# Performance work log

Measured on AMD Instinct MI355X. Metric: run time of the kernel, lower is better.

## Reference

```python
import jax, jax.numpy as jnp
from jax import lax
import numpy as np

EPS = 1e-5


def ref_points(Hk, Wk):
    # torch linspace(0.5, Hk-0.5, Hk)/Hk * 2 - 1, stacked (y, x)
    ys = (jnp.linspace(0.5, Hk - 0.5, Hk) / Hk) * 2.0 - 1.0
    xs = (jnp.linspace(0.5, Wk - 0.5, Wk) / Wk) * 2.0 - 1.0
    yy, xx = jnp.meshgrid(ys, xs, indexing='ij')
    return jnp.stack([yy, xx], axis=-1)  # (Hk, Wk, 2) in (y, x) order


def grid_sample(img, grid):
    # Bilinear, align_corners=True, zeros padding (torch F.grid_sample defaults).
    # img: (N, C, Hi, Wi); grid: (N, Hg, Wg, 2) with (x, y) in [-1, 1].
    N, C, Hi, Wi = img.shape
    Hg, Wg = grid.shape[1], grid.shape[2]
    gx = (grid[..., 0] + 1.0) * 0.5 * (Wi - 1)
    gy = (grid[..., 1] + 1.0) * 0.5 * (Hi - 1)
    x0 = jnp.floor(gx)
    y0 = jnp.floor(gy)
    wx1 = gx - x0
    wy1 = gy - y0
    imgf = img.reshape(N, C, Hi * Wi)

    def corner(ix, iy, w):
        valid = (ix >= 0) & (ix < Wi) & (iy >= 0) & (iy < Hi)
        idx = (jnp.clip(iy, 0, Hi - 1).astype(jnp.int32) * Wi
               + jnp.clip(ix, 0, Wi - 1).astype(jnp.int32)).reshape(N, -1)
        vals = jax.vmap(lambda im, f: im[:, f])(imgf, idx)  # (N, C, Hg*Wg)
        return vals * (w * valid).reshape(N, 1, -1)

    out = (corner(x0, y0, (1 - wx1) * (1 - wy1))
           + corner(x0 + 1, y0, wx1 * (1 - wy1))
           + corner(x0, y0 + 1, (1 - wx1) * wy1)
           + corner(x0 + 1, y0 + 1, wx1 * wy1))
    return out.reshape(N, C, Hg, Wg)


def setup_inputs() -> dict:
    key = jax.random.key(0)
    ks = jax.random.split(key, 8)
    B, C, H, W = 8, 128, 64, 64
    gc, nH = 64, 4
    return {
        'x': jax.random.normal(ks[0], (B, C, H, W), jnp.float32),
        'w_dw': jax.random.normal(ks[1], (gc, 1, 5, 5), jnp.float32) * 0.1,
        'ln_w': jnp.ones((gc,), jnp.float32),
        'w_off': jax.random.normal(ks[2], (3, gc), jnp.float32) * 0.1,
        'wq': jax.random.normal(ks[3], (C, C), jnp.float32) * 0.05,
        'wk': jax.random.normal(ks[4], (C, C), jnp.float32) * 0.05,
        'wv': jax.random.normal(ks[5], (C, C), jnp.float32) * 0.05,
        'wo': jax.random.normal(ks[6], (C, C), jnp.float32) * 0.05,
        'rpe': jax.random.normal(ks[7], (nH, 2 * H - 1, 2 * W - 1), jnp.float32) * 0.01,
    }


def reference(x, w_dw, ln_w, w_off, wq, wk, wv, wo, rpe):
    B, C, H, W = x.shape
    G, nH = 2, 4
    gc = C // G           # group channels
    dh = C // nH          # head channels
    gh = nH // G          # heads per group
    scale = dh ** -0.5
    orf = 1.0             # offset_range_factor

    conv1x1 = lambda t, w: jnp.einsum('oi,bihw->bohw', w, t)

    q = conv1x1(x, wq)                                    # (B, C, H, W)
    q_off = q.reshape(B * G, gc, H, W)

    # conv_offset: depthwise 5x5 stride 4 pad 2 -> BiasFree LN (over C) -> GELU -> 1x1 to 3
    off = lax.conv_general_dilated(q_off, w_dw, (4, 4), ((2, 2), (2, 2)),
                                   dimension_numbers=('NCHW', 'OIHW', 'NCHW'),
                                   feature_group_count=gc)  # (B*G, gc, Hk, Wk)
    var = jnp.var(off, axis=1, keepdims=True)
    off = off / jnp.sqrt(var + EPS) * ln_w.reshape(1, -1, 1, 1)
    off = jax.nn.gelu(off, approximate=False)
    off = jnp.einsum('oi,bihw->bohw', w_off, off)          # (B*G, 3, Hk, Wk)

    Hk, Wk = off.shape[2], off.shape[3]
    n = Hk * Wk

    # channel 0 = y offset, channel 1 = x offset, channel 2 = modulation
    offset = jnp.stack([jnp.tanh(off[:, 0]) * (orf / Hk),
                        jnp.tanh(off[:, 1]) * (orf / Wk)], axis=-1)  # (B*G, Hk, Wk, 2) (y,x)
    dm = jax.nn.sigmoid(off[:, 2])[:, None]                # (B*G, 1, Hk, Wk)

    pos = offset + ref_points(Hk, Wk)[None]                # (B*G, Hk, Wk, 2) (y,x)

    xs = grid_sample(x.reshape(B * G, gc, H, W), pos[..., ::-1])  # grid in (x,y)
    xs = (xs * dm).reshape(B, C, 1, n)

    k = conv1x1(xs, wk).reshape(B * nH, dh, n)
    v = conv1x1(xs, wv).reshape(B * nH, dh, n)
    qf = q.reshape(B * nH, dh, H * W)

    attn = jnp.einsum('bcm,bcn->bmn', qf, k) * scale       # (B*nH, H*W, n)

    # relative-position bias sampled at continuous displacements
    rpe_b = jnp.broadcast_to(rpe[None], (B, nH, 2 * H - 1, 2 * W - 1)
                             ).reshape(B * G, gh, 2 * H - 1, 2 * W - 1)
    qg = ref_points(H, W).reshape(H * W, 2)                # (H*W, 2)
    disp = (qg[None, :, None, :] - pos.reshape(B * G, 1, n, 2)) * 0.5  # (B*G, H*W, n, 2)
    bias = grid_sample(rpe_b, disp[..., ::-1]).reshape(B * nH, H * W, n)

    attn = jax.nn.softmax(attn + bias, axis=2)
    out = jnp.einsum('bmn,bcn->bcm', attn, v).reshape(B, C, H, W)
    return conv1x1(out, wo)
```

## Files before the change

kernel.cpp:

```cpp
#include <hip/hip_runtime.h>
#include <hip/hip_bf16.h>
#include <math.h>

#define HW 4096
#define NCH 128

typedef __attribute__((ext_vector_type(8))) short short8;
typedef __attribute__((ext_vector_type(4))) float f32x4;
typedef __attribute__((ext_vector_type(4))) unsigned u32x4;

__device__ __forceinline__ short f2bf(float f) {
  union { __hip_bfloat16 h; short s; } u;
  u.h = __float2bfloat16(f);
  return u.s;
}
__device__ __forceinline__ float bf2f(short s) {
  union { unsigned u; float f; } u;
  u.u = ((unsigned)(unsigned short)s) << 16;
  return u.f;
}

__global__ __launch_bounds__(256) void xq_kernel(
    const float* __restrict__ x, const float* __restrict__ wq,
    short* __restrict__ xT, float* __restrict__ qT) {
  __shared__ float s[128][65];
  int tid = threadIdx.x;
  int b = blockIdx.y;
  int m0 = blockIdx.x * 64;
  {
    int ml = tid & 63, ch = tid >> 6;
#pragma unroll
    for (int i = 0; i < 32; ++i) {
      int c = i * 4 + ch;
      s[c][ml] = x[((size_t)(b * NCH + c)) * HW + m0 + ml];
    }
  }
  __syncthreads();
  {
    int c = tid & 127, mh = tid >> 7;
#pragma unroll
    for (int i = 0; i < 32; ++i) {
      int m = i * 2 + mh;
      xT[((size_t)(b * HW + m0 + m)) * NCH + c] = f2bf(s[c][m]);
    }
  }
  int w = tid >> 6, lane = tid & 63, l15 = lane & 15, qd = lane >> 4;
  int mrow = w * 16 + l15;
  f32x4 acc[8];
#pragma unroll
  for (int ot = 0; ot < 8; ++ot) acc[ot] = (f32x4){0.f, 0.f, 0.f, 0.f};
#pragma unroll
  for (int kc = 0; kc < 4; ++kc) {
    short8 ah, al;
#pragma unroll
    for (int j = 0; j < 8; ++j) {
      float v = s[kc * 32 + qd * 8 + j][mrow];
      short hi = f2bf(v);
      ah[j] = hi;
      al[j] = f2bf(v - bf2f(hi));
    }
#pragma unroll
    for (int ot = 0; ot < 8; ++ot) {
      const float* wr = wq + (size_t)(ot * 16 + l15) * NCH + kc * 32 + qd * 8;
      f32x4 w0 = *(const f32x4*)wr;
      f32x4 w1 = *(const f32x4*)(wr + 4);
      short8 bh, bl;
#pragma unroll
      for (int j = 0; j < 4; ++j) {
        short h0 = f2bf(w0[j]);
        bh[j] = h0;
        bl[j] = f2bf(w0[j] - bf2f(h0));
        short h1 = f2bf(w1[j]);
        bh[4 + j] = h1;
        bl[4 + j] = f2bf(w1[j] - bf2f(h1));
      }
      acc[ot] = __builtin_amdgcn_mfma_f32_16x16x32_bf16(ah, bh, acc[ot], 0, 0, 0);
      acc[ot] = __builtin_amdgcn_mfma_f32_16x16x32_bf16(al, bh, acc[ot], 0, 0, 0);
      acc[ot] = __builtin_amdgcn_mfma_f32_16x16x32_bf16(ah, bl, acc[ot], 0, 0, 0);
    }
  }
#pragma unroll
  for (int ot = 0; ot < 8; ++ot)
#pragma unroll
    for (int r = 0; r < 4; ++r)
      qT[((size_t)(b * HW + m0 + w * 16 + qd * 4 + r)) * NCH + ot * 16 + l15] =
          acc[ot][r];
}

__device__ __forceinline__ float wsum64(float v) {
#pragma unroll
  for (int o = 32; o > 0; o >>= 1) v += __shfl_xor(v, o);
  return v;
}

__global__ __launch_bounds__(256) void conv_offset_kernel(
    const float* __restrict__ qT, const float* __restrict__ w_dw,
    const float* __restrict__ ln_w, const float* __restrict__ w_off,
    const float* __restrict__ wk, const float* __restrict__ wv,
    const float* __restrict__ wo, const float* __restrict__ rpe,
    float* __restrict__ pos, float* __restrict__ dm,
    short* __restrict__ wk_bf, short* __restrict__ wv_bf,
    short* __restrict__ wo_bf, unsigned* __restrict__ tab) {
  int tid = threadIdx.x;
  if (blockIdx.x >= 64) {
    int id = (blockIdx.x - 64) * 16 + blockIdx.y;
    if (id < 64) {
      int i = id * 256 + tid;
      wk_bf[i] = f2bf(wk[i]);
      wv_bf[i] = f2bf(wv[i]);
      wo_bf[i] = f2bf(wo[i]);
    } else {
      int i = (id - 64) * 256 + tid;
      int h = i >> 14, r = i & 16383;
      int row = r >> 7, col = r & 127;
      float lo = 0.f, hi = 0.f;
      if (col < 127) {
        if (row >= 1) lo = rpe[h * 16129 + (row - 1) * 127 + col];
        if (row < 127) hi = rpe[h * 16129 + row * 127 + col];
      }
      union { unsigned u; _Float16 h2[2]; } pk;
      pk.h2[0] = (_Float16)(lo * 1.4426950408889634f);
      pk.h2[1] = (_Float16)(hi * 1.4426950408889634f);
      tab[i] = pk.u;
    }
    return;
  }
  int c = tid & 63;
  int p = blockIdx.x * 4 + (tid >> 6);
  int bg = blockIdx.y;
  int py = p >> 4, px = p & 15;
  const float* qp = qT + (size_t)(bg >> 1) * HW * NCH + (bg & 1) * 64 + c;
  const float* wd = w_dw + c * 25;
  float acc = 0.f;
#pragma unroll
  for (int ky = 0; ky < 5; ++ky) {
    int iy = 4 * py + ky - 2;
    if (iy < 0 || iy >= 64) continue;
#pragma unroll
    for (int kx = 0; kx < 5; ++kx) {
      int ix = 4 * px + kx - 2;
      if (ix < 0 || ix >= 64) continue;
      acc += wd[ky * 5 + kx] * qp[(size_t)(iy * 64 + ix) * NCH];
    }
  }
  float mean = wsum64(acc) * (1.f / 64.f);
  float msq = wsum64(acc * acc) * (1.f / 64.f);
  float var = msq - mean * mean;
  float g = acc * rsqrtf(var + 1e-5f) * ln_w[c];
  g = 0.5f * g * (1.f + erff(g * 0.70710678118654752f));
  float o0 = wsum64(w_off[c] * g);
  float o1 = wsum64(w_off[64 + c] * g);
  float o2 = wsum64(w_off[128 + c] * g);
  if (c == 0) {
    int idx = bg * 256 + p;
    pos[idx * 2] = tanhf(o0) * (1.f / 16.f) + ((py + 0.5f) * (1.f / 8.f) - 1.f);
    pos[idx * 2 + 1] = tanhf(o1) * (1.f / 16.f) + ((px + 0.5f) * (1.f / 8.f) - 1.f);
    dm[idx] = 1.f / (1.f + expf(-o2));
  }
}

__global__ __launch_bounds__(256) void sample_xs_kernel(
    const short* __restrict__ xT, const float* __restrict__ pos,
    const float* __restrict__ dm, short* __restrict__ xsT) {
  int tid = threadIdx.x;
  int c = tid & 63;
  int p = blockIdx.y * 4 + (tid >> 6);
  int bg = blockIdx.x;
  int b = bg >> 1, ch0 = (bg & 1) * 64;
  int idx = bg * 256 + p;
  float posy = pos[idx * 2], posx = pos[idx * 2 + 1];
  float dmv = dm[idx];
  float gx = (posx + 1.f) * 31.5f;
  float gy = (posy + 1.f) * 31.5f;
  float x0f = floorf(gx), y0f = floorf(gy);
  int ix = (int)x0f, iy = (int)y0f;
  float fx = gx - x0f, fy = gy - y0f;
  float w00 = (1.f - fx) * (1.f - fy), w10 = fx * (1.f - fy);
  float w01 = (1.f - fx) * fy, w11 = fx * fy;
  bool vx0 = (ix >= 0 && ix < 64), vx1 = (ix + 1 >= 0 && ix + 1 < 64);
  bool vy0 = (iy >= 0 && iy < 64), vy1 = (iy + 1 >= 0 && iy + 1 < 64);
  if (!(vx0 && vy0)) w00 = 0.f;
  if (!(vx1 && vy0)) w10 = 0.f;
  if (!(vx0 && vy1)) w01 = 0.f;
  if (!(vx1 && vy1)) w11 = 0.f;
  int x0c = min(max(ix, 0), 63), x1c = min(max(ix + 1, 0), 63);
  int y0c = min(max(iy, 0), 63), y1c = min(max(iy + 1, 0), 63);
  size_t rb = (size_t)b * HW * NCH + ch0 + c;
  float v = w00 * bf2f(xT[rb + (size_t)(y0c * 64 + x0c) * NCH]) +
            w10 * bf2f(xT[rb + (size_t)(y0c * 64 + x1c) * NCH]) +
            w01 * bf2f(xT[rb + (size_t)(y1c * 64 + x0c) * NCH]) +
            w11 * bf2f(xT[rb + (size_t)(y1c * 64 + x1c) * NCH]);
  xsT[((size_t)(b * 256 + p)) * NCH + ch0 + c] = f2bf(v * dmv);
}

__global__ __launch_bounds__(256) void kv_mfma_kernel(
    const short* __restrict__ xsT, const short* __restrict__ wk_bf,
    const short* __restrict__ wv_bf, short* __restrict__ kbf,
    short* __restrict__ vbf) {
  int tid = threadIdx.x;
  int w = tid >> 6, lane = tid & 63, l15 = lane & 15, qd = lane >> 4;
  int bh = blockIdx.x, b = bh >> 2;
  int n0 = blockIdx.y * 64 + w * 16;
  f32x4 acc[2];
  acc[0] = (f32x4){0.f, 0.f, 0.f, 0.f};
  acc[1] = (f32x4){0.f, 0.f, 0.f, 0.f};

  size_t xrow = ((size_t)(b * 256 + n0 + l15)) * NCH + qd * 8;
  if (blockIdx.z == 0) {
#pragma unroll
    for (int kc = 0; kc < 4; ++kc) {
      short8 a = *(const short8*)&xsT[xrow + kc * 32];
#pragma unroll
      for (int ot = 0; ot < 2; ++ot) {
        short8 bb = *(const short8*)&wk_bf[(size_t)((bh & 3) * 32 + ot * 16 + l15) * NCH + kc * 32 + qd * 8];
        acc[ot] = __builtin_amdgcn_mfma_f32_16x16x32_bf16(a, bb, acc[ot], 0, 0, 0);
      }
    }
#pragma unroll
    for (int ot = 0; ot < 2; ++ot)
#pragma unroll
      for (int r = 0; r < 4; ++r)
        kbf[((size_t)(bh * 256 + n0 + qd * 4 + r)) * 32 + ot * 16 + l15] =
            f2bf(acc[ot][r]);
  } else {
#pragma unroll
    for (int kc = 0; kc < 4; ++kc) {
      short8 bb = *(const short8*)&xsT[xrow + kc * 32];
#pragma unroll
      for (int ot = 0; ot < 2; ++ot) {
        short8 a = *(const short8*)&wv_bf[(size_t)((bh & 3) * 32 + ot * 16 + l15) * NCH + kc * 32 + qd * 8];
        acc[ot] = __builtin_amdgcn_mfma_f32_16x16x32_bf16(a, bb, acc[ot], 0, 0, 0);
      }
    }
#pragma unroll
    for (int ot = 0; ot < 2; ++ot)
#pragma unroll
      for (int r = 0; r < 4; ++r)
        vbf[((size_t)(bh * 32 + ot * 16 + qd * 4 + r)) * 256 + n0 + l15] =
            f2bf(acc[ot][r]);
  }
}

#define PROW 264
#define TROWS 72

__global__ __launch_bounds__(256, 4) void attn_kernel(
    const float* __restrict__ qT, const short* __restrict__ kbf,
    const short* __restrict__ vbf, const float* __restrict__ pos,
    const unsigned* __restrict__ tabg, short* __restrict__ outT) {
  __shared__ __align__(16) unsigned s_tab[TROWS * 128];
  __shared__ __align__(16) float s_pxs[256];
  __shared__ __align__(16) unsigned s_fy[256];
  __shared__ __align__(16) unsigned s_row[256];
  short* s_p = (short*)s_tab;

  int tid = threadIdx.x;
  int wv = tid >> 6;
  int lane = tid & 63;
  int l15 = lane & 15;
  int qd = lane >> 4;
  int bh = blockIdx.y;
  int b = bh >> 2, h = bh & 3;
  int bg = b * 2 + (h >> 1);
  int m0 = blockIdx.x * 64 + wv * 16;

  float ry = ((float)blockIdx.x + 0.5f) * (1.f / 32.f) - 1.f;
  float gy0 = 63.f + ry * 31.5f;
  int row0 = min(max((int)floorf(gy0) - 34, 0), 128 - TROWS);

  {
    const uint4* src = (const uint4*)(tabg + (size_t)h * 16384 + row0 * 128);
    uint4* dst = (uint4*)s_tab;
#pragma unroll
    for (int i = 0; i < 9; ++i)
      __builtin_amdgcn_global_load_lds(
          (const __attribute__((address_space(1))) void*)(src + i * 256 + tid),
          (__attribute__((address_space(3))) void*)(dst + i * 256 + tid), 16,
          0, 0);
  }
  {
    float2 p2 = ((const float2*)(pos + (size_t)bg * 512))[tid];
    float gyb = gy0 - (float)row0 + 1.f;
    float gy = gyb - p2.x * 31.5f;
    float y0f = floorf(gy);
    union { unsigned u; _Float16 h2[2]; } pk;
    pk.h2[0] = (_Float16)(gy - y0f);
    pk.h2[1] = (_Float16)0.f;
    s_pxs[tid] = p2.y * 31.5f;
    s_fy[tid] = pk.u;
    s_row[tid] = ((unsigned)(int)y0f) << 7;
  }

  short8 qfrag;
  {
    const float* qg = qT + ((size_t)(b * HW + m0 + l15)) * NCH + h * 32 + qd * 8;
    f32x4 a0 = *(const f32x4*)qg;
    f32x4 a1 = *(const f32x4*)(qg + 4);
#pragma unroll
    for (int j = 0; j < 4; ++j) {
      qfrag[j] = f2bf(a0[j]);
      qfrag[4 + j] = f2bf(a1[j]);
    }
  }

  f32x4 acc[16];
  {
    const short* kb = kbf + ((size_t)bh * 256 + l15) * 32 + qd * 8;
#pragma unroll
    for (int t = 0; t < 16; ++t) {
      short8 kf = *(const short8*)(kb + t * 16 * 32);
      acc[t] = __builtin_amdgcn_mfma_f32_16x16x32_bf16(
          kf, qfrag, (f32x4){0.f, 0.f, 0.f, 0.f}, 0, 0, 0);
    }
  }
  __syncthreads();

  int m = m0 + l15;
  float gx0 = ((((float)(m & 63) + 0.5f) * (1.f / 32.f) - 1.f) * 0.5f + 1.f) * 63.f;
  float mx = -1e30f;
#pragma unroll
  for (int t = 0; t < 16; ++t) {
    int nb = t * 16 + qd * 4;
    f32x4 pxs4 = *(const f32x4*)&s_pxs[nb];
    u32x4 fy4 = *(const u32x4*)&s_fy[nb];
    u32x4 rw4 = *(const u32x4*)&s_row[nb];
#pragma unroll
    for (int r = 0; r < 4; ++r) {
      float gx = gx0 - pxs4[r];
      float x0f = floorf(gx);
      float fx = gx - x0f;
      int xl = (int)x0f;
      int rowi = (int)rw4[r];
      unsigned left = s_tab[rowi + (xl & 127)];
      unsigned right = s_tab[rowi + xl + 1];
      union { unsigned u; _Float16 h2[2]; } L, R, F;
      L.u = left;
      R.u = right;
      F.u = fy4[r];
      _Float16 fy16 = F.h2[0];
      _Float16 bL = (_Float16)(L.h2[0] + fy16 * (L.h2[1] - L.h2[0]));
      _Float16 bR = (_Float16)(R.h2[0] + fy16 * (R.h2[1] - R.h2[0]));
      float bLf = (float)bL, bRf = (float)bR;
      float bias = bLf + fx * (bRf - bLf);
      float s = fmaf(acc[t][r], 0.25503486121880191f, bias);
      acc[t][r] = s;
      mx = fmaxf(mx, s);
    }
  }
  mx = fmaxf(mx, __shfl_xor(mx, 16));
  float M = fmaxf(mx, __shfl_xor(mx, 32));

  float sm = 0.f;
#pragma unroll
  for (int t = 0; t < 16; ++t) {
#pragma unroll
    for (int r = 0; r < 4; ++r) {
      float e = exp2f(acc[t][r] - M);
      acc[t][r] = e;
      sm += e;
    }
  }
  sm += __shfl_xor(sm, 16);
  sm += __shfl_xor(sm, 32);
  float inv = 1.f / sm;

  __syncthreads();

  {
    short* pw = s_p + wv * 16 * PROW + l15 * PROW;
#pragma unroll
    for (int t = 0; t < 16; ++t) {
      int n = t * 16 + qd * 4;
      short4 pk;
      pk.x = f2bf(acc[t][0]);
      pk.y = f2bf(acc[t][1]);
      pk.z = f2bf(acc[t][2]);
      pk.w = f2bf(acc[t][3]);
      *(short4*)(pw + n) = pk;
    }
  }

  f32x4 o0 = {0.f, 0.f, 0.f, 0.f}, o1 = {0.f, 0.f, 0.f, 0.f};
  {
    const short* vb = vbf + ((size_t)bh * 32 + l15) * 256 + qd * 8;
    const short* pr = s_p + wv * 16 * PROW + l15 * PROW + qd * 8;
#pragma unroll
    for (int ch = 0; ch < 8; ++ch) {
      short8 pf = *(const short8*)(pr + ch * 32);
      short8 v0 = *(const short8*)(vb + ch * 32);
      short8 v1 = *(const short8*)(vb + 16 * 256 + ch * 32);
      o0 = __builtin_amdgcn_mfma_f32_16x16x32_bf16(v0, pf, o0, 0, 0, 0);
      o1 = __builtin_amdgcn_mfma_f32_16x16x32_bf16(v1, pf, o1, 0, 0, 0);
    }
  }
  {
    size_t row = (size_t)(b * HW + m0 + l15) * NCH + h * 32 + qd * 4;
    short4 s0, s1;
    s0.x = f2bf(o0[0] * inv); s0.y = f2bf(o0[1] * inv);
    s0.z = f2bf(o0[2] * inv); s0.w = f2bf(o0[3] * inv);
    s1.x = f2bf(o1[0] * inv); s1.y = f2bf(o1[1] * inv);
    s1.z = f2bf(o1[2] * inv); s1.w = f2bf(o1[3] * inv);
    *(short4*)&outT[row] = s0;
    *(short4*)&outT[row + 16] = s1;
  }
}

__global__ __launch_bounds__(256) void wo_mfma_kernel(
    const short* __restrict__ attnT, const short* __restrict__ wo_bf,
    float* __restrict__ out) {
  int tid = threadIdx.x;
  int wv = tid >> 6;
  int lane = tid & 63;
  int l15 = lane & 15;
  int qd = lane >> 4;
  int b = blockIdx.x >> 6;
  int m0 = (blockIdx.x & 63) * 64 + wv * 16;

  f32x4 acc[8];
#pragma unroll
  for (int ot = 0; ot < 8; ++ot) acc[ot] = (f32x4){0.f, 0.f, 0.f, 0.f};

  const short* arow = attnT + (size_t)(b * HW + m0 + l15) * NCH + qd * 8;
  const short* wrow = wo_bf + (size_t)l15 * NCH + qd * 8;
#pragma unroll
  for (int kc = 0; kc < 4; ++kc) {
    short8 afrag = *(const short8*)(arow + kc * 32);
#pragma unroll
    for (int ot = 0; ot < 8; ++ot) {
      short8 bfrag = *(const short8*)(wrow + (size_t)ot * 16 * NCH + kc * 32);
      acc[ot] = __builtin_amdgcn_mfma_f32_16x16x32_bf16(afrag, bfrag, acc[ot],
                                                        0, 0, 0);
    }
  }
#pragma unroll
  for (int ot = 0; ot < 8; ++ot) {
    float* op = out + ((size_t)b * NCH + ot * 16 + l15) * HW + m0 + qd * 4;
    *(f32x4*)op = acc[ot];
  }
}

extern "C" void kernel_launch(void* const* d_in, const int* in_sizes, int n_in,
                              void* d_out, int out_size, void* d_ws,
                              size_t ws_size, hipStream_t stream) {
  const float* x = (const float*)d_in[0];
  const float* w_dw = (const float*)d_in[1];
  const float* ln_w = (const float*)d_in[2];
  const float* w_off = (const float*)d_in[3];
  const float* wq = (const float*)d_in[4];
  const float* wk = (const float*)d_in[5];
  const float* wv = (const float*)d_in[6];
  const float* wo = (const float*)d_in[7];
  const float* rpe = (const float*)d_in[8];
  float* out = (float*)d_out;

  float* qT = out;
  short* sb = (short*)d_ws;
  short* xT = sb;
  short* outT = sb;
  short* xsT = sb + 4194304;
  short* kbf = sb + 4456448;
  short* vbf = sb + 4718592;
  short* wk_bf = sb + 4980736;
  short* wv_bf = sb + 4997120;
  short* wo_bf = sb + 5013504;
  unsigned* tab = (unsigned*)(sb + 5029888);
  float* pos = (float*)(sb + 5160960);
  float* dm = pos + 8192;

  xq_kernel<<<dim3(64, 8), 256, 0, stream>>>(x, wq, xT, qT);
  conv_offset_kernel<<<dim3(84, 16), 256, 0, stream>>>(
      qT, w_dw, ln_w, w_off, wk, wv, wo, rpe, pos, dm, wk_bf, wv_bf, wo_bf,
      tab);
  sample_xs_kernel<<<dim3(16, 64), 256, 0, stream>>>(xT, pos, dm, xsT);
  kv_mfma_kernel<<<dim3(32, 4, 2), 256, 0, stream>>>(xsT, wk_bf, wv_bf, kbf,
                                                     vbf);
  attn_kernel<<<dim3(64, 32), 256, 0, stream>>>(qT, kbf, vbf, pos, tab, outT);
  wo_mfma_kernel<<<512, 256, 0, stream>>>(outT, wo_bf, out);
}
```

Before: 167.7 us.

## Fuse sampling with K/V projection and move weight prep into Q kernel

Merges the bilinear sampling of x and the K/V projection into one kernel that stages the sampled tile in shared memory, so the xsT round trip through global memory and one launch go away. The weight bf16 conversion and rpe table build move from the conv-offset kernel into extra blocks of the Q-projection kernel. In the attention kernel the two table reads are merged into one packed 8-byte load. The fused sample/KV grid has only 32 blocks of 512 threads, which may leave most of the GPU idle. The packed load also drops the &127 wrap on the left index.

```diff
diff --git a/kernel.cpp b/kernel.cpp
--- a/kernel.cpp
+++ b/kernel.cpp
@@ -22,88 +22,15 @@
 
 __global__ __launch_bounds__(256) void xq_kernel(
     const float* __restrict__ x, const float* __restrict__ wq,
-    short* __restrict__ xT, float* __restrict__ qT) {
+    const float* __restrict__ wk, const float* __restrict__ wv,
+    const float* __restrict__ wo, const float* __restrict__ rpe,
+    short* __restrict__ xT, float* __restrict__ qT,
+    short* __restrict__ wk_bf, short* __restrict__ wv_bf,
+    short* __restrict__ wo_bf, unsigned* __restrict__ tab) {
   __shared__ float s[128][65];
   int tid = threadIdx.x;
-  int b = blockIdx.y;
-  int m0 = blockIdx.x * 64;
-  {
-    int ml = tid & 63, ch = tid >> 6;
-#pragma unroll
-    for (int i = 0; i < 32; ++i) {
-      int c = i * 4 + ch;
-      s[c][ml] = x[((size_t)(b * NCH + c)) * HW + m0 + ml];
-    }
-  }
-  __syncthreads();
-  {
-    int c = tid & 127, mh = tid >> 7;
-#pragma unroll
-    for (int i = 0; i < 32; ++i) {
-      int m = i * 2 + mh;
-      xT[((size_t)(b * HW + m0 + m)) * NCH + c] = f2bf(s[c][m]);
-    }
-  }
-  int w = tid >> 6, lane = tid & 63, l15 = lane & 15, qd = lane >> 4;
-  int mrow = w * 16 + l15;
-  f32x4 acc[8];
-#pragma unroll
-  for (int ot = 0; ot < 8; ++ot) acc[ot] = (f32x4){0.f, 0.f, 0.f, 0.f};
-#pragma unroll
-  for (int kc = 0; kc < 4; ++kc) {
-    short8 ah, al;
-#pragma unroll
-    for (int j = 0; j < 8; ++j) {
-      float v = s[kc * 32 + qd * 8 + j][mrow];
-      short hi = f2bf(v);
-      ah[j] = hi;
-      al[j] = f2bf(v - bf2f(hi));
-    }
-#pragma unroll
-    for (int ot = 0; ot < 8; ++ot) {
-      const float* wr = wq + (size_t)(ot * 16 + l15) * NCH + kc * 32 + qd * 8;
-      f32x4 w0 = *(const f32x4*)wr;
-      f32x4 w1 = *(const f32x4*)(wr + 4);
-      short8 bh, bl;
-#pragma unroll
-      for (int j = 0; j < 4; ++j) {
-        short h0 = f2bf(w0[j]);
-        bh[j] = h0;
-        bl[j] = f2bf(w0[j] - bf2f(h0));
-        short h1 = f2bf(w1[j]);
-        bh[4 + j] = h1;
-        bl[4 + j] = f2bf(w1[j] - bf2f(h1));
-      }
-      acc[ot] = __builtin_amdgcn_mfma_f32_16x16x32_bf16(ah, bh, acc[ot], 0, 0, 0);
-      acc[ot] = __builtin_amdgcn_mfma_f32_16x16x32_bf16(al, bh, acc[ot], 0, 0, 0);
-      acc[ot] = __builtin_amdgcn_mfma_f32_16x16x32_bf16(ah, bl, acc[ot], 0, 0, 0);
-    }
-  }
-#pragma unroll
-  for (int ot = 0; ot < 8; ++ot)
-#pragma unroll
-    for (int r = 0; r < 4; ++r)
-      qT[((size_t)(b * HW + m0 + w * 16 + qd * 4 + r)) * NCH + ot * 16 + l15] =
-          acc[ot][r];
-}
-
-__device__ __forceinline__ float wsum64(float v) {
-#pragma unroll
-  for (int o = 32; o > 0; o >>= 1) v += __shfl_xor(v, o);
-  return v;
-}
-
-__global__ __launch_bounds__(256) void conv_offset_kernel(
-    const float* __restrict__ qT, const float* __restrict__ w_dw,
-    const float* __restrict__ ln_w, const float* __restrict__ w_off,
-    const float* __restrict__ wk, const float* __restrict__ wv,
-    const float* __restrict__ wo, const float* __restrict__ rpe,
-    float* __restrict__ pos, float* __restrict__ dm,
-    short* __restrict__ wk_bf, short* __restrict__ wv_bf,
-    short* __restrict__ wo_bf, unsigned* __restrict__ tab) {
-  int tid = threadIdx.x;
-  if (blockIdx.x >= 64) {
-    int id = (blockIdx.x - 64) * 16 + blockIdx.y;
+  if (blockIdx.y >= 8) {
+    int id = (blockIdx.y - 8) * 64 + blockIdx.x;
     if (id < 64) {
       int i = id * 256 + tid;
       wk_bf[i] = f2bf(wk[i]);
@@ -125,6 +52,79 @@
     }
     return;
   }
+  int b = blockIdx.y;
+  int m0 = blockIdx.x * 64;
+  {
+    int ml = tid & 63, ch = tid >> 6;
+#pragma unroll
+    for (int i = 0; i < 32; ++i) {
+      int c = i * 4 + ch;
+      s[c][ml] = x[((size_t)(b * NCH + c)) * HW + m0 + ml];
+    }
+  }
+  __syncthreads();
+  {
+    int c = tid & 127, mh = tid >> 7;
+#pragma unroll
+    for (int i = 0; i < 32; ++i) {
+      int m = i * 2 + mh;
+      xT[((size_t)(b * HW + m0 + m)) * NCH + c] = f2bf(s[c][m]);
+    }
+  }
+  int w = tid >> 6, lane = tid & 63, l15 = lane & 15, qd = lane >> 4;
+  int mrow = w * 16 + l15;
+  f32x4 acc[8];
+#pragma unroll
+  for (int ot = 0; ot < 8; ++ot) acc[ot] = (f32x4){0.f, 0.f, 0.f, 0.f};
+#pragma unroll
+  for (int kc = 0; kc < 4; ++kc) {
+    short8 ah, al;
+#pragma unroll
+    for (int j = 0; j < 8; ++j) {
+      float v = s[kc * 32 + qd * 8 + j][mrow];
+      short hi = f2bf(v);
+      ah[j] = hi;
+      al[j] = f2bf(v - bf2f(hi));
+    }
+#pragma unroll
+    for (int ot = 0; ot < 8; ++ot) {
+      const float* wr = wq + (size_t)(ot * 16 + l15) * NCH + kc * 32 + qd * 8;
+      f32x4 w0 = *(const f32x4*)wr;
+      f32x4 w1 = *(const f32x4*)(wr + 4);
+      short8 bh, bl;
+#pragma unroll
+      for (int j = 0; j < 4; ++j) {
+        short h0 = f2bf(w0[j]);
+        bh[j] = h0;
+        bl[j] = f2bf(w0[j] - bf2f(h0));
+        short h1 = f2bf(w1[j]);
+        bh[4 + j] = h1;
+        bl[4 + j] = f2bf(w1[j] - bf2f(h1));
+      }
+      acc[ot] = __builtin_amdgcn_mfma_f32_16x16x32_bf16(ah, bh, acc[ot], 0, 0, 0);
+      acc[ot] = __builtin_amdgcn_mfma_f32_16x16x32_bf16(al, bh, acc[ot], 0, 0, 0);
+      acc[ot] = __builtin_amdgcn_mfma_f32_16x16x32_bf16(ah, bl, acc[ot], 0, 0, 0);
+    }
+  }
+#pragma unroll
+  for (int ot = 0; ot < 8; ++ot)
+#pragma unroll
+    for (int r = 0; r < 4; ++r)
+      qT[((size_t)(b * HW + m0 + w * 16 + qd * 4 + r)) * NCH + ot * 16 + l15] =
+          acc[ot][r];
+}
+
+__device__ __forceinline__ float wsum64(float v) {
+#pragma unroll
+  for (int o = 32; o > 0; o >>= 1) v += __shfl_xor(v, o);
+  return v;
+}
+
+__global__ __launch_bounds__(256) void conv_offset_kernel(
+    const float* __restrict__ qT, const float* __restrict__ w_dw,
+    const float* __restrict__ ln_w, const float* __restrict__ w_off,
+    float* __restrict__ pos, float* __restrict__ dm) {
+  int tid = threadIdx.x;
   int c = tid & 63;
   int p = blockIdx.x * 4 + (tid >> 6);
   int bg = blockIdx.y;
@@ -159,90 +159,104 @@
   }
 }
 
-__global__ __launch_bounds__(256) void sample_xs_kernel(
+#define XSROW 136
+
+__global__ __launch_bounds__(512) void sample_kv_kernel(
     const short* __restrict__ xT, const float* __restrict__ pos,
-    const float* __restrict__ dm, short* __restrict__ xsT) {
-  int tid = threadIdx.x;
-  int c = tid & 63;
-  int p = blockIdx.y * 4 + (tid >> 6);
-  int bg = blockIdx.x;
-  int b = bg >> 1, ch0 = (bg & 1) * 64;
-  int idx = bg * 256 + p;
-  float posy = pos[idx * 2], posx = pos[idx * 2 + 1];
-  float dmv = dm[idx];
-  float gx = (posx + 1.f) * 31.5f;
-  float gy = (posy + 1.f) * 31.5f;
-  float x0f = floorf(gx), y0f = floorf(gy);
-  int ix = (int)x0f, iy = (int)y0f;
-  float fx = gx - x0f, fy = gy - y0f;
-  float w00 = (1.f - fx) * (1.f - fy), w10 = fx * (1.f - fy);
-  float w01 = (1.f - fx) * fy, w11 = fx * fy;
-  bool vx0 = (ix >= 0 && ix < 64), vx1 = (ix + 1 >= 0 && ix + 1 < 64);
-  bool vy0 = (iy >= 0 && iy < 64), vy1 = (iy + 1 >= 0 && iy + 1 < 64);
-  if (!(vx0 && vy0)) w00 = 0.f;
-  if (!(vx1 && vy0)) w10 = 0.f;
-  if (!(vx0 && vy1)) w01 = 0.f;
-  if (!(vx1 && vy1)) w11 = 0.f;
-  int x0c = min(max(ix, 0), 63), x1c = min(max(ix + 1, 0), 63);
-  int y0c = min(max(iy, 0), 63), y1c = min(max(iy + 1, 0), 63);
-  size_t rb = (size_t)b * HW * NCH + ch0 + c;
-  float v = w00 * bf2f(xT[rb + (size_t)(y0c * 64 + x0c) * NCH]) +
-            w10 * bf2f(xT[rb + (size_t)(y0c * 64 + x1c) * NCH]) +
-            w01 * bf2f(xT[rb + (size_t)(y1c * 64 + x0c) * NCH]) +
-            w11 * bf2f(xT[rb + (size_t)(y1c * 64 + x1c) * NCH]);
-  xsT[((size_t)(b * 256 + p)) * NCH + ch0 + c] = f2bf(v * dmv);
-}
-
-__global__ __launch_bounds__(256) void kv_mfma_kernel(
-    const short* __restrict__ xsT, const short* __restrict__ wk_bf,
+    const float* __restrict__ dm, const short* __restrict__ wk_bf,
     const short* __restrict__ wv_bf, short* __restrict__ kbf,
     short* __restrict__ vbf) {
+  __shared__ __align__(16) short s_xs[64 * XSROW];
   int tid = threadIdx.x;
-  int w = tid >> 6, lane = tid & 63, l15 = lane & 15, qd = lane >> 4;
-  int bh = blockIdx.x, b = bh >> 2;
-  int n0 = blockIdx.y * 64 + w * 16;
-  f32x4 acc[2];
-  acc[0] = (f32x4){0.f, 0.f, 0.f, 0.f};
-  acc[1] = (f32x4){0.f, 0.f, 0.f, 0.f};
-
-  size_t xrow = ((size_t)(b * 256 + n0 + l15)) * NCH + qd * 8;
-  if (blockIdx.z == 0) {
-#pragma unroll
-    for (int kc = 0; kc < 4; ++kc) {
-      short8 a = *(const short8*)&xsT[xrow + kc * 32];
+  int w = tid >> 6, lane = tid & 63;
+  int b = blockIdx.x, nblk = blockIdx.y;
+  int n0 = nblk * 64;
+
+#pragma unroll
+  for (int j = 0; j < 16; ++j) {
+    int tsk = w * 16 + j;
+    int p_loc = tsk >> 1, hf = tsk & 1;
+    int idx = (b * 2 + hf) * 256 + n0 + p_loc;
+    float posy = pos[idx * 2], posx = pos[idx * 2 + 1];
+    float dmv = dm[idx];
+    float gx = (posx + 1.f) * 31.5f;
+    float gy = (posy + 1.f) * 31.5f;
+    float x0f = floorf(gx), y0f = floorf(gy);
+    int ix = (int)x0f, iy = (int)y0f;
+    float fx = gx - x0f, fy = gy - y0f;
+    float w00 = (1.f - fx) * (1.f - fy), w10 = fx * (1.f - fy);
+    float w01 = (1.f - fx) * fy, w11 = fx * fy;
+    bool vx0 = (ix >= 0 && ix < 64), vx1 = (ix + 1 >= 0 && ix + 1 < 64);
+    bool vy0 = (iy >= 0 && iy < 64), vy1 = (iy + 1 >= 0 && iy + 1 < 64);
+    if (!(vx0 && vy0)) w00 = 0.f;
+    if (!(vx1 && vy0)) w10 = 0.f;
+    if (!(vx0 && vy1)) w01 = 0.f;
+    if (!(vx1 && vy1)) w11 = 0.f;
+    int x0c = min(max(ix, 0), 63), x1c = min(max(ix + 1, 0), 63);
+    int y0c = min(max(iy, 0), 63), y1c = min(max(iy + 1, 0), 63);
+    size_t rb = (size_t)b * HW * NCH + hf * 64 + lane;
+    float v = w00 * bf2f(xT[rb + (size_t)(y0c * 64 + x0c) * NCH]) +
+              w10 * bf2f(xT[rb + (size_t)(y0c * 64 + x1c) * NCH]) +
+              w01 * bf2f(xT[rb + (size_t)(y1c * 64 + x0c) * NCH]) +
+              w11 * bf2f(xT[rb + (size_t)(y1c * 64 + x1c) * NCH]);
+    s_xs[p_loc * XSROW + hf * 64 + lane] = f2bf(v * dmv);
+  }
+  __syncthreads();
+
+  int l15 = lane & 15, qd = lane >> 4;
+  int hw = w & 3;
+  int bh = b * 4 + hw;
+#pragma unroll
+  for (int mt = 0; mt < 4; ++mt) {
+    f32x4 a0 = (f32x4){0.f, 0.f, 0.f, 0.f};
+    f32x4 a1 = (f32x4){0.f, 0.f, 0.f, 0.f};
+    const short* xr = s_xs + (mt * 16 + l15) * XSROW + qd * 8;
+    if (w < 4) {
+#pragma unroll
+      for (int kc = 0; kc < 4; ++kc) {
+        short8 a = *(const short8*)(xr + kc * 32);
+#pragma unroll
+        for (int ot = 0; ot < 2; ++ot) {
+          short8 bb = *(const short8*)&wk_bf[(size_t)(hw * 32 + ot * 16 + l15) * NCH + kc * 32 + qd * 8];
+          f32x4& ac = ot ? a1 : a0;
+          ac = __builtin_amdgcn_mfma_f32_16x16x32_bf16(a, bb, ac, 0, 0, 0);
+        }
+      }
 #pragma unroll
       for (int ot = 0; ot < 2; ++ot) {
-        short8 bb = *(const short8*)&wk_bf[(size_t)((bh & 3) * 32 + ot * 16 + l15) * NCH + kc * 32 + qd * 8];
-        acc[ot] = __builtin_amdgcn_mfma_f32_16x16x32_bf16(a, bb, acc[ot], 0, 0, 0);
-      }
-    }
-#pragma unroll
-    for (int ot = 0; ot < 2; ++ot)
-#pragma unroll
-      for (int r = 0; r < 4; ++r)
-        kbf[((size_t)(bh * 256 + n0 + qd * 4 + r)) * 32 + ot * 16 + l15] =
-            f2bf(acc[ot][r]);
-  } else {
-#pragma unroll
-    for (int kc = 0; kc < 4; ++kc) {
-      short8 bb = *(const short8*)&xsT[xrow + kc * 32];
+        f32x4& ac = ot ? a1 : a0;
+#pragma unroll
+        for (int r = 0; r < 4; ++r)
+          kbf[((size_t)(bh * 256 + n0 + mt * 16 + qd * 4 + r)) * 32 + ot * 16 + l15] =
+              f2bf(ac[r]);
+      }
+    } else {
+#pragma unroll
+      for (int kc = 0; kc < 4; ++kc) {
+        short8 bb = *(const short8*)(xr + kc * 32);
+#pragma unroll
+        for (int ot = 0; ot < 2; ++ot) {
+          short8 a = *(const short8*)&wv_bf[(size_t)(hw * 32 + ot * 16 + l15) * NCH + kc * 32 + qd * 8];
+          f32x4& ac = ot ? a1 : a0;
+          ac = __builtin_amdgcn_mfma_f32_16x16x32_bf16(a, bb, ac, 0, 0, 0);
+        }
+      }
 #pragma unroll
       for (int ot = 0; ot < 2; ++ot) {
-        short8 a = *(const short8*)&wv_bf[(size_t)((bh & 3) * 32 + ot * 16 + l15) * NCH + kc * 32 + qd * 8];
-        acc[ot] = __builtin_amdgcn_mfma_f32_16x16x32_bf16(a, bb, acc[ot], 0, 0, 0);
-      }
-    }
-#pragma unroll
-    for (int ot = 0; ot < 2; ++ot)
-#pragma unroll
-      for (int r = 0; r < 4; ++r)
-        vbf[((size_t)(bh * 32 + ot * 16 + qd * 4 + r)) * 256 + n0 + l15] =
-            f2bf(acc[ot][r]);
+        f32x4& ac = ot ? a1 : a0;
+#pragma unroll
+        for (int r = 0; r < 4; ++r)
+          vbf[((size_t)(bh * 32 + ot * 16 + qd * 4 + r)) * 256 + n0 + mt * 16 + l15] =
+              f2bf(ac[r]);
+      }
+    }
   }
 }
 
 #define PROW 264
 #define TROWS 72
+
+struct __attribute__((packed)) upair { unsigned lo, hi; };
 
 __global__ __launch_bounds__(256, 4) void attn_kernel(
     const float* __restrict__ qT, const short* __restrict__ kbf,
@@ -330,12 +344,11 @@
       float x0f = floorf(gx);
       float fx = gx - x0f;
       int xl = (int)x0f;
-      int rowi = (int)rw4[r];
-      unsigned left = s_tab[rowi + (xl & 127)];
-      unsigned right = s_tab[rowi + xl + 1];
+      int ai = (int)rw4[r] + xl;
+      upair pr = *(const upair*)(s_tab + ai);
       union { unsigned u; _Float16 h2[2]; } L, R, F;
-      L.u = left;
-      R.u = right;
+      L.u = pr.lo;
+      R.u = pr.hi;
       F.u = fy4[r];
       _Float16 fy16 = F.h2[0];
       _Float16 bL = (_Float16)(L.h2[0] + fy16 * (L.h2[1] - L.h2[0]));
@@ -457,7 +470,6 @@
   short* sb = (short*)d_ws;
   short* xT = sb;
   short* outT = sb;
-  short* xsT = sb + 4194304;
   short* kbf = sb + 4456448;
   short* vbf = sb + 4718592;
   short* wk_bf = sb + 4980736;
@@ -467,13 +479,12 @@
   float* pos = (float*)(sb + 5160960);
   float* dm = pos + 8192;
 
-  xq_kernel<<<dim3(64, 8), 256, 0, stream>>>(x, wq, xT, qT);
-  conv_offset_kernel<<<dim3(84, 16), 256, 0, stream>>>(
-      qT, w_dw, ln_w, w_off, wk, wv, wo, rpe, pos, dm, wk_bf, wv_bf, wo_bf,
-      tab);
-  sample_xs_kernel<<<dim3(16, 64), 256, 0, stream>>>(xT, pos, dm, xsT);
-  kv_mfma_kernel<<<dim3(32, 4, 2), 256, 0, stream>>>(xsT, wk_bf, wv_bf, kbf,
-                                                     vbf);
+  xq_kernel<<<dim3(64, 13), 256, 0, stream>>>(x, wq, wk, wv, wo, rpe, xT, qT,
+                                              wk_bf, wv_bf, wo_bf, tab);
+  conv_offset_kernel<<<dim3(64, 16), 256, 0, stream>>>(qT, w_dw, ln_w, w_off,
+                                                       pos, dm);
+  sample_kv_kernel<<<dim3(8, 4), 512, 0, stream>>>(xT, pos, dm, wk_bf, wv_bf,
+                                                   kbf, vbf);
   attn_kernel<<<dim3(64, 32), 256, 0, stream>>>(qT, kbf, vbf, pos, tab, outT);
   wo_mfma_kernel<<<512, 256, 0, stream>>>(outT, wo_bf, out);
 }
```

Result: slower. 174.7 us (+4.2%).
